# Kernel optimization log

Hardware: AMD Instinct MI355X
Metric: run time of the kernel (lower is better)

## Reference

```python
import jax, jax.numpy as jnp
import numpy as np

BATCH, LENGTH = 4, 512
D_MODEL, D_STATE, EXPAND = 128, 256, 2
D_INNER = EXPAND * D_MODEL  # 256 (== D_STATE, required by the original broadcasting)


def setup_inputs() -> dict:
    key = jax.random.key(0)
    ks = jax.random.split(key, 8)
    x = jax.random.normal(ks[0], (BATCH, LENGTH, D_MODEL), jnp.float32)
    # bias-free Dense kernels, fan-in scaled; W_delta and A kept small so
    # exp(delta*A)^L stays numerically tame over L=512 steps.
    W_in = jax.random.normal(ks[1], (D_MODEL, 2 * D_INNER), jnp.float32) / np.float32(np.sqrt(D_MODEL))
    W_delta = jax.random.normal(ks[2], (D_INNER, D_INNER), jnp.float32) * np.float32(0.005)
    W_B = jax.random.normal(ks[3], (D_INNER, D_STATE), jnp.float32) / np.float32(np.sqrt(D_INNER))
    W_C = jax.random.normal(ks[4], (D_INNER, D_INNER), jnp.float32) / np.float32(np.sqrt(D_INNER))
    W_out = jax.random.normal(ks[5], (D_INNER, D_MODEL), jnp.float32) / np.float32(np.sqrt(D_INNER))
    A = jax.random.normal(ks[6], (D_INNER, D_STATE), jnp.float32) * np.float32(0.02)
    D = jnp.ones((D_INNER,), jnp.float32)  # unused by the original scan, kept for faithfulness
    return dict(x=x, W_in=W_in, W_delta=W_delta, W_B=W_B, W_C=W_C, W_out=W_out, A=A, D=D)


def reference(x, W_in, W_delta, W_B, W_C, W_out, A, D):
    # in_proj + split
    x_proj = x @ W_in                      # (b, l, 2*d_inner)
    xs, z = jnp.split(x_proj, 2, axis=-1)  # each (b, l, d_inner)
    delta = xs @ W_delta                   # (b, l, d_inner)
    Bv = xs @ W_B                          # (b, l, d_state)
    Cv = xs @ W_C                          # (b, l, d_inner)

    # discretized transition/input, exactly as the original einsums
    deltaA = jnp.exp(jnp.einsum('bld,dn->bldn', delta, A))   # (b, l, d_inner, d_state)
    deltaB = jnp.einsum('bld,bln->bldn', delta, Bv)          # (b, l, d_inner, d_state)

    def step(state, inp):
        dA_i, dB_i, x_i, C_i = inp
        # state: (b, d_inner, d_state); x broadcast over the middle axis as in tf.expand_dims(x,1)
        state = dA_i * state + dB_i * x_i[:, None, :]
        y = jnp.einsum('bdn,bn->bd', state, C_i)
        return state, y

    init = jnp.zeros((x.shape[0], D_INNER, D_STATE), xs.dtype)
    inps = (
        jnp.moveaxis(deltaA, 1, 0),  # (l, b, d, n)
        jnp.moveaxis(deltaB, 1, 0),
        jnp.moveaxis(xs, 1, 0),      # (l, b, d)
        jnp.moveaxis(Cv, 1, 0),
    )
    _, ys = jax.lax.scan(step, init, inps)   # ys: (l, b, d_inner)
    y = jnp.moveaxis(ys, 0, 1)               # (b, l, d_inner)

    y = y * jax.nn.silu(z)
    return y @ W_out                          # (b, l, d_model)
```

## Files before the change

kernel.cpp:

```cpp
#include <hip/hip_runtime.h>
#include <hip/hip_bf16.h>


#define MROWS 2048
#define DM 128
#define DI 256
#define DS 256
#define LLEN 512
#define LC 64
#define NC 8

#define LOG2E 1.44269504088896340736f

typedef short bf16x8 __attribute__((ext_vector_type(8)));
typedef float f32x4  __attribute__((ext_vector_type(4)));

__device__ __forceinline__ short f2bf(float f) {
    union { float f; unsigned u; } v; v.f = f;
    unsigned r = v.u + 0x7FFFu + ((v.u >> 16) & 1u);
    return (short)(r >> 16);
}

#define TEXP2(c1, c2, dl) fmaf(fmaf((c2), (dl), (c1)), (dl), 1.f)

__device__ __forceinline__ void tconv(float (*tile)[33],
                                      const float* __restrict__ src,
                                      short* __restrict__ dst,
                                      int Ms, int Ns, int ti, int tj, int tid)
{
    const int r = tid >> 5, c = tid & 31;
#pragma unroll
    for (int i = 0; i < 4; ++i)
        tile[r + 8 * i][c] = src[(size_t)(ti * 32 + r + 8 * i) * Ns + tj * 32 + c];
    __syncthreads();
#pragma unroll
    for (int i = 0; i < 4; ++i)
        dst[(size_t)(tj * 32 + r + 8 * i) * Ms + ti * 32 + c] = f2bf(tile[c][r + 8 * i]);
}

__global__ __launch_bounds__(256) void k_proj_mfma(
    const float* __restrict__ x, const float* __restrict__ W_in,
    const float* __restrict__ Wd, const float* __restrict__ Wb,
    const float* __restrict__ Wc, const float* __restrict__ W_out,
    float* __restrict__ xs, short* __restrict__ xs_bf, float* __restrict__ sz,
    short* __restrict__ WdbcT, short* __restrict__ W_outT)
{
    const int t = threadIdx.x;

    if (blockIdx.x >= 8) {
        __shared__ float tile[32][33];
        const int uu = (blockIdx.x - 8) * 32 + blockIdx.y;
        if (uu < 64)       tconv(tile, Wd,    WdbcT,                       256, 256, uu & 7,         uu >> 3,         t);
        else if (uu < 128) tconv(tile, Wb,    WdbcT + (size_t)256 * 256,   256, 256, (uu - 64) & 7,  (uu - 64) >> 3,  t);
        else if (uu < 192) tconv(tile, Wc,    WdbcT + (size_t)512 * 256,   256, 256, (uu - 128) & 7, (uu - 128) >> 3, t);
        else if (uu < 224) tconv(tile, W_out, W_outT,                      256, 128, (uu - 192) & 7, (uu - 192) >> 3, t);
        return;
    }

    __shared__ short As[64][136];
    __shared__ short Bs[64][136];
    f32x4 acc[4] = {};
    const int w = t >> 6, lane = t & 63;
    const int srow = t >> 2, sseg = t & 3;
    const int frow = lane & 15, fk = (lane >> 4) << 3;
    const int r0 = blockIdx.y * 64, n0 = blockIdx.x * 64;

    {
        const float* ap = x + (size_t)(r0 + srow) * DM + sseg * 32;
        short tmp[32];
#pragma unroll
        for (int j = 0; j < 8; ++j) {
            float4 f = *(const float4*)(ap + j * 4);
            tmp[j * 4 + 0] = f2bf(f.x); tmp[j * 4 + 1] = f2bf(f.y);
            tmp[j * 4 + 2] = f2bf(f.z); tmp[j * 4 + 3] = f2bf(f.w);
        }
#pragma unroll
        for (int m = 0; m < 4; ++m)
            *(bf16x8*)&As[srow][sseg * 32 + m * 8] = *(bf16x8*)&tmp[m * 8];
    }
    {
#pragma unroll
        for (int i = 0; i < 32; i += 2) {
            const int k = sseg * 32 + i;
            float f0 = W_in[(size_t)k * 512 + n0 + srow];
            float f1 = W_in[(size_t)(k + 1) * 512 + n0 + srow];
            unsigned pk = (unsigned short)f2bf(f0) | ((unsigned)(unsigned short)f2bf(f1) << 16);
            *(unsigned*)&Bs[srow][k] = pk;
        }
    }
    __syncthreads();

#pragma unroll
    for (int kk = 0; kk < 128; kk += 32) {
        bf16x8 af = *(const bf16x8*)&As[w * 16 + frow][kk + fk];
#pragma unroll
        for (int ct = 0; ct < 4; ++ct) {
            bf16x8 bfr = *(const bf16x8*)&Bs[ct * 16 + frow][kk + fk];
            acc[ct] = __builtin_amdgcn_mfma_f32_16x16x32_bf16(af, bfr, acc[ct], 0, 0, 0);
        }
    }

    const int rr = r0 + w * 16 + (lane >> 4) * 4;
    const int c0 = n0 + (lane & 15);
#pragma unroll
    for (int ct = 0; ct < 4; ++ct) {
        const int c = c0 + ct * 16;
#pragma unroll
        for (int rg = 0; rg < 4; ++rg) {
            const float v = acc[ct][rg];
            const int r = rr + rg;
            if (c < DI) {
                xs[(size_t)r * DI + c]    = v;
                xs_bf[(size_t)r * DI + c] = f2bf(v);
            } else {
                sz[(size_t)r * DI + (c - DI)] = v / (1.f + __expf(-v));
            }
        }
    }
}

__global__ __launch_bounds__(512) void k_dbc(
    const short* __restrict__ xs_bf, const short* __restrict__ WdbcT,
    const float* __restrict__ xs,
    float* __restrict__ dlt, float* __restrict__ u, float* __restrict__ cvv)
{
    __shared__ short As[64][72], Bs[128][72];
    const int blk = blockIdx.x, t = threadIdx.x;
    const int w8 = t >> 6, lane = t & 63;
    const int rf = w8 & 3, ch = w8 >> 2;
    const int frow = lane & 15, fk = (lane >> 4) << 3;
    const int bx = blk % 6, by = blk / 6;
    const int r0 = by * 64, n0 = bx * 128;
    const int arow = t >> 3, ak = (t & 7) * 8;
    const int brow = t >> 2, bk = (t & 3) * 16;
    f32x4 acc[4] = {};

    for (int k0 = 0; k0 < DI; k0 += 64) {
        bf16x8 a0 = *(const bf16x8*)(xs_bf + (size_t)(r0 + arow) * DI + k0 + ak);
        bf16x8 b0 = *(const bf16x8*)(WdbcT + (size_t)(n0 + brow) * DI + k0 + bk);
        bf16x8 b1 = *(const bf16x8*)(WdbcT + (size_t)(n0 + brow) * DI + k0 + bk + 8);
        __syncthreads();
        *(bf16x8*)&As[arow][ak]     = a0;
        *(bf16x8*)&Bs[brow][bk]     = b0;
        *(bf16x8*)&Bs[brow][bk + 8] = b1;
        __syncthreads();
#pragma unroll
        for (int kk = 0; kk < 64; kk += 32) {
            bf16x8 af = *(const bf16x8*)&As[rf * 16 + frow][kk + fk];
#pragma unroll
            for (int ct = 0; ct < 4; ++ct) {
                bf16x8 bfr = *(const bf16x8*)&Bs[(ch * 4 + ct) * 16 + frow][kk + fk];
                acc[ct] = __builtin_amdgcn_mfma_f32_16x16x32_bf16(af, bfr, acc[ct], 0, 0, 0);
            }
        }
    }

    const int rr = r0 + rf * 16 + (lane >> 4) * 4;
    const int nbase = n0 + ch * 64;
    const int wsel = nbase >> 8;
    const int nb = nbase & 255;
#pragma unroll
    for (int ct = 0; ct < 4; ++ct) {
        const int c = nb + ct * 16 + (lane & 15);
#pragma unroll
        for (int rg = 0; rg < 4; ++rg) {
            const float v = acc[ct][rg];
            const size_t idx = (size_t)(rr + rg) * DI + c;
            if (wsel == 0)      dlt[idx] = v;
            else if (wsel == 1) u[idx]   = v * xs[idx];
            else                cvv[idx] = v;
        }
    }
}

__global__ __launch_bounds__(256) void k_scan1(
    const float* __restrict__ dlt, const float* __restrict__ u,
    const float* __restrict__ Aa,
    float* __restrict__ tc, float* __restrict__ dsm)
{
    const int lane = threadIdx.x & 63;
    const int w    = threadIdx.x >> 6;
    const int blk  = blockIdx.x;
    const int b  = blk & 3;
    const int c  = (blk >> 2) & 7;
    const int d0 = ((blk >> 5) * 4 + w) * 4;

    __shared__ float dls[4][4][LC];
    const size_t base = (size_t)b * LLEN * DI + (size_t)c * LC * DI;

    float4 dv = *(const float4*)(dlt + base + (size_t)lane * DI + d0);
    dls[w][0][lane] = dv.x;
    dls[w][1][lane] = dv.y;
    dls[w][2][lane] = dv.z;
    dls[w][3][lane] = dv.w;
    float dsv[4] = { dv.x, dv.y, dv.z, dv.w };
#pragma unroll
    for (int dd = 0; dd < 4; ++dd) {
#pragma unroll
        for (int off = 32; off > 0; off >>= 1)
            dsv[dd] += __shfl_xor(dsv[dd], off);
    }

    float4 c1[4], c2[4];
#pragma unroll
    for (int dd = 0; dd < 4; ++dd) {
        float4 a = *(const float4*)(Aa + (size_t)(d0 + dd) * DS + lane * 4);
        c1[dd] = a;
        c2[dd] = make_float4(0.5f * a.x * a.x, 0.5f * a.y * a.y,
                             0.5f * a.z * a.z, 0.5f * a.w * a.w);
    }

    const float4* up = (const float4*)(u + base) + lane;
    float4 s[4] = {};
    float4 uA[4], uB[4];

#define S1_PRE(UB, G)                                                         \
    {                                                                         \
        _Pragma("unroll")                                                     \
        for (int i = 0; i < 4; ++i)                                           \
            UB[i] = up[(size_t)((G) * 4 + i) * 64];                           \
    }

#define S1_COMP(UB, G)                                                        \
    {                                                                         \
        _Pragma("unroll")                                                     \
        for (int i = 0; i < 4; ++i) {                                         \
            const int l = (G) * 4 + i;                                        \
            _Pragma("unroll")                                                 \
            for (int dd = 0; dd < 4; ++dd) {                                  \
                const float dl = dls[w][dd][l];                               \
                s[dd].x = fmaf(TEXP2(c1[dd].x, c2[dd].x, dl), s[dd].x, dl * UB[i].x); \
                s[dd].y = fmaf(TEXP2(c1[dd].y, c2[dd].y, dl), s[dd].y, dl * UB[i].y); \
                s[dd].z = fmaf(TEXP2(c1[dd].z, c2[dd].z, dl), s[dd].z, dl * UB[i].z); \
                s[dd].w = fmaf(TEXP2(c1[dd].w, c2[dd].w, dl), s[dd].w, dl * UB[i].w); \
            }                                                                 \
        }                                                                     \
    }

    S1_PRE(uA, 0)
    for (int g2 = 0; g2 < 8; ++g2) {
        S1_PRE(uB, g2 * 2 + 1)
        S1_COMP(uA, g2 * 2)
        if (g2 < 7) S1_PRE(uA, g2 * 2 + 2)
        S1_COMP(uB, g2 * 2 + 1)
    }
#undef S1_PRE
#undef S1_COMP

    const size_t rbb = ((size_t)(b * 256 + d0)) * NC + c;
#pragma unroll
    for (int dd = 0; dd < 4; ++dd) {
        *(float4*)(tc + (rbb + (size_t)dd * NC) * 256 + lane * 4) = s[dd];
        if (lane == 0) dsm[rbb + dd * NC] = dsv[dd];
    }
}

__global__ __launch_bounds__(256) void k_scan3(
    const float* __restrict__ dlt, const float* __restrict__ u,
    const float* __restrict__ cvv, const float* __restrict__ Aa,
    const float* __restrict__ tc, const float* __restrict__ dsm,
    float* __restrict__ yv)
{
    const int lane = threadIdx.x & 63;
    const int w    = threadIdx.x >> 6;
    const int blk  = blockIdx.x;
    const int b  = blk & 3;
    const int c  = (blk >> 2) & 7;
    const int d0 = ((blk >> 5) * 4 + w) * 4;

    __shared__ float dls[4][4][LC];
    __shared__ float T[4][LC][20];

    const size_t base = (size_t)b * LLEN * DI + (size_t)c * LC * DI;

    float4 dv = *(const float4*)(dlt + base + (size_t)lane * DI + d0);
    dls[w][0][lane] = dv.x;
    dls[w][1][lane] = dv.y;
    dls[w][2][lane] = dv.z;
    dls[w][3][lane] = dv.w;

    float4 c1[4], c2[4];
#pragma unroll
    for (int dd = 0; dd < 4; ++dd) {
        float4 a = *(const float4*)(Aa + (size_t)(d0 + dd) * DS + lane * 4);
        c1[dd] = a;
        c2[dd] = make_float4(0.5f * a.x * a.x, 0.5f * a.y * a.y,
                             0.5f * a.z * a.z, 0.5f * a.w * a.w);
    }

    float4 s[4] = {};
    for (int cc = 0; cc < c; ++cc) {
#pragma unroll
        for (int dd = 0; dd < 4; ++dd) {
            const size_t rbd = ((size_t)(b * 256 + d0 + dd)) * NC + cc;
            const float4 Tt = *(const float4*)(tc + rbd * 256 + lane * 4);
            const float  Dc = dsm[rbd] * LOG2E;
            s[dd].x = exp2f(c1[dd].x * Dc) * s[dd].x + Tt.x;
            s[dd].y = exp2f(c1[dd].y * Dc) * s[dd].y + Tt.y;
            s[dd].z = exp2f(c1[dd].z * Dc) * s[dd].z + Tt.z;
            s[dd].w = exp2f(c1[dd].w * Dc) * s[dd].w + Tt.w;
        }
    }

    const float4* up = (const float4*)(u + base) + lane;
    const float4* cp = (const float4*)(cvv + base) + lane;
    float* yb = yv + base;

    const int col = lane & 15, seg = lane >> 4;
    float4 uA[4], cA[4], uB[4], cB[4];

#define S3_PRE(UB, CB, G)                                                     \
    {                                                                         \
        _Pragma("unroll")                                                     \
        for (int i = 0; i < 4; ++i) {                                         \
            UB[i] = up[(size_t)((G) * 4 + i) * 64];                           \
            CB[i] = cp[(size_t)((G) * 4 + i) * 64];                           \
        }                                                                     \
    }

#define S3_COMP(UB, CB, G)                                                    \
    {                                                                         \
        f32x4 pacc[4];                                                        \
        _Pragma("unroll")                                                     \
        for (int i = 0; i < 4; ++i) {                                         \
            const int l = (G) * 4 + i;                                        \
            _Pragma("unroll")                                                 \
            for (int dd = 0; dd < 4; ++dd) {                                  \
                const float dl = dls[w][dd][l];                               \
                s[dd].x = fmaf(TEXP2(c1[dd].x, c2[dd].x, dl), s[dd].x, dl * UB[i].x); \
                s[dd].y = fmaf(TEXP2(c1[dd].y, c2[dd].y, dl), s[dd].y, dl * UB[i].y); \
                s[dd].z = fmaf(TEXP2(c1[dd].z, c2[dd].z, dl), s[dd].z, dl * UB[i].z); \
                s[dd].w = fmaf(TEXP2(c1[dd].w, c2[dd].w, dl), s[dd].w, dl * UB[i].w); \
                pacc[dd][i] =                                                 \
                    fmaf(s[dd].w, CB[i].w, fmaf(s[dd].z, CB[i].z,             \
                         fmaf(s[dd].y, CB[i].y, s[dd].x * CB[i].x)));         \
            }                                                                 \
        }                                                                     \
        _Pragma("unroll")                                                     \
        for (int dd = 0; dd < 4; ++dd)                                        \
            *(f32x4*)&T[w][lane][dd * 4] = pacc[dd];                          \
        float sm = 0.f;                                                       \
        _Pragma("unroll")                                                     \
        for (int r = 0; r < 16; ++r)                                          \
            sm += T[w][seg * 16 + r][col];                                    \
        sm += __shfl_xor(sm, 16);                                             \
        sm += __shfl_xor(sm, 32);                                             \
        if (lane < 16)                                                        \
            yb[(size_t)((G) * 4 + (col & 3)) * DI + d0 + (col >> 2)] = sm;    \
    }

    S3_PRE(uA, cA, 0)
    for (int g2 = 0; g2 < 8; ++g2) {
        S3_PRE(uB, cB, g2 * 2 + 1)
        S3_COMP(uA, cA, g2 * 2)
        if (g2 < 7) S3_PRE(uA, cA, g2 * 2 + 2)
        S3_COMP(uB, cB, g2 * 2 + 1)
    }
#undef S3_PRE
#undef S3_COMP
}

__global__ __launch_bounds__(256) void k_out_mfma(
    const float* __restrict__ y, const float* __restrict__ szp,
    const short* __restrict__ W_outT, float* __restrict__ out)
{
    __shared__ short As[64][72], Bs[64][72];
    f32x4 acc[4] = {};
    const int tid  = threadIdx.x;
    const int w    = tid >> 6, lane = tid & 63;
    const int srow = tid >> 2, sseg = tid & 3;
    const int frow = lane & 15, fk = (lane >> 4) << 3;
    const int r0 = blockIdx.y * 64, n0 = blockIdx.x * 64;

    for (int k0 = 0; k0 < DI; k0 += 64) {
        const size_t aoff = (size_t)(r0 + srow) * DI + k0 + sseg * 16;
        float4 y0 = *(const float4*)(y + aoff);
        float4 y1 = *(const float4*)(y + aoff + 4);
        float4 y2 = *(const float4*)(y + aoff + 8);
        float4 y3 = *(const float4*)(y + aoff + 12);
        float4 s0 = *(const float4*)(szp + aoff);
        float4 s1 = *(const float4*)(szp + aoff + 4);
        float4 s2 = *(const float4*)(szp + aoff + 8);
        float4 s3 = *(const float4*)(szp + aoff + 12);
        const short* bg = W_outT + (size_t)(n0 + srow) * DI + k0 + sseg * 16;
        bf16x8 b0 = *(const bf16x8*)bg;
        bf16x8 b1 = *(const bf16x8*)(bg + 8);
        bf16x8 a0, a1;
        a0[0] = f2bf(y0.x * s0.x); a0[1] = f2bf(y0.y * s0.y);
        a0[2] = f2bf(y0.z * s0.z); a0[3] = f2bf(y0.w * s0.w);
        a0[4] = f2bf(y1.x * s1.x); a0[5] = f2bf(y1.y * s1.y);
        a0[6] = f2bf(y1.z * s1.z); a0[7] = f2bf(y1.w * s1.w);
        a1[0] = f2bf(y2.x * s2.x); a1[1] = f2bf(y2.y * s2.y);
        a1[2] = f2bf(y2.z * s2.z); a1[3] = f2bf(y2.w * s2.w);
        a1[4] = f2bf(y3.x * s3.x); a1[5] = f2bf(y3.y * s3.y);
        a1[6] = f2bf(y3.z * s3.z); a1[7] = f2bf(y3.w * s3.w);
        __syncthreads();
        *(bf16x8*)&As[srow][sseg * 16]     = a0;
        *(bf16x8*)&As[srow][sseg * 16 + 8] = a1;
        *(bf16x8*)&Bs[srow][sseg * 16]     = b0;
        *(bf16x8*)&Bs[srow][sseg * 16 + 8] = b1;
        __syncthreads();
#pragma unroll
        for (int kk = 0; kk < 64; kk += 32) {
            bf16x8 af = *(const bf16x8*)&As[w * 16 + frow][kk + fk];
#pragma unroll
            for (int ct = 0; ct < 4; ++ct) {
                bf16x8 bfr = *(const bf16x8*)&Bs[ct * 16 + frow][kk + fk];
                acc[ct] = __builtin_amdgcn_mfma_f32_16x16x32_bf16(af, bfr, acc[ct], 0, 0, 0);
            }
        }
    }

    const int rr = r0 + w * 16 + (lane >> 4) * 4;
    const int c0 = n0 + (lane & 15);
#pragma unroll
    for (int ct = 0; ct < 4; ++ct) {
        const int c = c0 + ct * 16;
#pragma unroll
        for (int rg = 0; rg < 4; ++rg)
            out[(size_t)(rr + rg) * DM + c] = acc[ct][rg];
    }
}

extern "C" void kernel_launch(void* const* d_in, const int* in_sizes, int n_in,
                              void* d_out, int out_size, void* d_ws, size_t ws_size,
                              hipStream_t stream)
{
    const float* x       = (const float*)d_in[0];
    const float* W_in    = (const float*)d_in[1];
    const float* W_delta = (const float*)d_in[2];
    const float* W_B     = (const float*)d_in[3];
    const float* W_C     = (const float*)d_in[4];
    const float* W_out   = (const float*)d_in[5];
    const float* A       = (const float*)d_in[6];

    float* out = (float*)d_out;
    float* ws  = (float*)d_ws;

    const size_t S = (size_t)MROWS * DI;
    float* xs  = ws;
    float* sz  = ws + S;
    float* dlt = ws + 2 * S;
    float* u   = ws + 3 * S;
    float* cv  = ws + 4 * S;
    float* yv  = ws + 5 * S;
    float* tc  = ws + 6 * S;
    float* dsm = tc + (size_t)1024 * NC * 256;

    short* xs_bf  = (short*)(dsm + (size_t)1024 * NC);
    short* WdbcT  = xs_bf + (size_t)MROWS * DI;
    short* W_outT = WdbcT + (size_t)768 * DI;

    k_proj_mfma<<<dim3(15, 32), 256, 0, stream>>>(x, W_in, W_delta, W_B, W_C, W_out,
                                                  xs, xs_bf, sz, WdbcT, W_outT);
    k_dbc      <<<dim3(192), 512, 0, stream>>>(xs_bf, WdbcT, xs, dlt, u, cv);
    k_scan1    <<<dim3(512), 256, 0, stream>>>(dlt, u, A, tc, dsm);
    k_scan3    <<<dim3(512), 256, 0, stream>>>(dlt, u, cv, A, tc, dsm, yv);
    k_out_mfma <<<dim3(2, 32), 256, 0, stream>>>(yv, sz, W_outT, out);
}
```

Measured before the change: 69.56 us.

## Fuse output projection into scan3 via last-block atomic counter, trim scan1 chunks

Drops the separate output-projection kernel. Each scan3 block bumps a per-(batch, chunk) atomic counter, and the 16th block to finish a chunk runs the gated bf16 MFMA projection for that chunk's 64 rows, reusing the T shared buffer as tiles. scan1 now launches 448 blocks covering only chunks 0-6, since the last chunk's carry summary is apparently unused, and scan1 resets the counters. This removes one launch and the kernel boundary, but the projection now runs on only a few tail blocks per chunk, serialising both output halves in one block, and it relies on the fences ordering yv correctly.

```diff
diff --git a/kernel.cpp b/kernel.cpp
--- a/kernel.cpp
+++ b/kernel.cpp
@@ -176,14 +176,18 @@
 __global__ __launch_bounds__(256) void k_scan1(
     const float* __restrict__ dlt, const float* __restrict__ u,
     const float* __restrict__ Aa,
-    float* __restrict__ tc, float* __restrict__ dsm)
+    float* __restrict__ tc, float* __restrict__ dsm,
+    unsigned* __restrict__ cnt)
 {
     const int lane = threadIdx.x & 63;
     const int w    = threadIdx.x >> 6;
     const int blk  = blockIdx.x;
     const int b  = blk & 3;
-    const int c  = (blk >> 2) & 7;
-    const int d0 = ((blk >> 5) * 4 + w) * 4;
+    const int r  = blk >> 2;
+    const int c  = r % 7;
+    const int d0 = ((r / 7) * 4 + w) * 4;
+
+    if (blk < 32 && threadIdx.x == 0) cnt[blk] = 0u;
 
     __shared__ float dls[4][4][LC];
     const size_t base = (size_t)b * LLEN * DI + (size_t)c * LC * DI;
@@ -259,7 +263,9 @@
     const float* __restrict__ dlt, const float* __restrict__ u,
     const float* __restrict__ cvv, const float* __restrict__ Aa,
     const float* __restrict__ tc, const float* __restrict__ dsm,
-    float* __restrict__ yv)
+    float* __restrict__ yv,
+    const float* __restrict__ szp, const short* __restrict__ W_outT,
+    float* __restrict__ out, unsigned* __restrict__ cnt)
 {
     const int lane = threadIdx.x & 63;
     const int w    = threadIdx.x >> 6;
@@ -270,6 +276,7 @@
 
     __shared__ float dls[4][4][LC];
     __shared__ float T[4][LC][20];
+    __shared__ bool  lastf;
 
     const size_t base = (size_t)b * LLEN * DI + (size_t)c * LC * DI;
 
@@ -358,67 +365,73 @@
     }
 #undef S3_PRE
 #undef S3_COMP
-}
-
-__global__ __launch_bounds__(256) void k_out_mfma(
-    const float* __restrict__ y, const float* __restrict__ szp,
-    const short* __restrict__ W_outT, float* __restrict__ out)
-{
-    __shared__ short As[64][72], Bs[64][72];
-    f32x4 acc[4] = {};
-    const int tid  = threadIdx.x;
-    const int w    = tid >> 6, lane = tid & 63;
-    const int srow = tid >> 2, sseg = tid & 3;
-    const int frow = lane & 15, fk = (lane >> 4) << 3;
-    const int r0 = blockIdx.y * 64, n0 = blockIdx.x * 64;
-
-    for (int k0 = 0; k0 < DI; k0 += 64) {
-        const size_t aoff = (size_t)(r0 + srow) * DI + k0 + sseg * 16;
-        float4 y0 = *(const float4*)(y + aoff);
-        float4 y1 = *(const float4*)(y + aoff + 4);
-        float4 y2 = *(const float4*)(y + aoff + 8);
-        float4 y3 = *(const float4*)(y + aoff + 12);
-        float4 s0 = *(const float4*)(szp + aoff);
-        float4 s1 = *(const float4*)(szp + aoff + 4);
-        float4 s2 = *(const float4*)(szp + aoff + 8);
-        float4 s3 = *(const float4*)(szp + aoff + 12);
-        const short* bg = W_outT + (size_t)(n0 + srow) * DI + k0 + sseg * 16;
-        bf16x8 b0 = *(const bf16x8*)bg;
-        bf16x8 b1 = *(const bf16x8*)(bg + 8);
-        bf16x8 a0, a1;
-        a0[0] = f2bf(y0.x * s0.x); a0[1] = f2bf(y0.y * s0.y);
-        a0[2] = f2bf(y0.z * s0.z); a0[3] = f2bf(y0.w * s0.w);
-        a0[4] = f2bf(y1.x * s1.x); a0[5] = f2bf(y1.y * s1.y);
-        a0[6] = f2bf(y1.z * s1.z); a0[7] = f2bf(y1.w * s1.w);
-        a1[0] = f2bf(y2.x * s2.x); a1[1] = f2bf(y2.y * s2.y);
-        a1[2] = f2bf(y2.z * s2.z); a1[3] = f2bf(y2.w * s2.w);
-        a1[4] = f2bf(y3.x * s3.x); a1[5] = f2bf(y3.y * s3.y);
-        a1[6] = f2bf(y3.z * s3.z); a1[7] = f2bf(y3.w * s3.w);
+
+    __threadfence();
+    if (threadIdx.x == 0)
+        lastf = (atomicAdd(&cnt[b * 8 + c], 1u) == 15u);
+    __syncthreads();
+    if (!lastf) return;
+    __threadfence();
+
+    short (*As)[72] = reinterpret_cast<short(*)[72]>(&T[0][0][0]);
+    short (*Bs)[72] = reinterpret_cast<short(*)[72]>(&T[0][0][0]) + 64;
+    const int r0f = b * 512 + c * 64;
+    const int t   = threadIdx.x;
+    const int ww  = t >> 6, ln = t & 63;
+    const int srow = t >> 2, sseg = t & 3;
+    const int frow = ln & 15, fk = (ln >> 4) << 3;
+
+    for (int half = 0; half < 2; ++half) {
+        const int n0 = half * 64;
+        f32x4 acc[4] = {};
+        for (int k0 = 0; k0 < DI; k0 += 64) {
+            const size_t aoff = (size_t)(r0f + srow) * DI + k0 + sseg * 16;
+            float4 y0 = *(const float4*)(yv + aoff);
+            float4 y1 = *(const float4*)(yv + aoff + 4);
+            float4 y2 = *(const float4*)(yv + aoff + 8);
+            float4 y3 = *(const float4*)(yv + aoff + 12);
+            float4 s0 = *(const float4*)(szp + aoff);
+            float4 s1 = *(const float4*)(szp + aoff + 4);
+            float4 s2 = *(const float4*)(szp + aoff + 8);
+            float4 s3 = *(const float4*)(szp + aoff + 12);
+            const short* bg = W_outT + (size_t)(n0 + srow) * DI + k0 + sseg * 16;
+            bf16x8 b0 = *(const bf16x8*)bg;
+            bf16x8 b1 = *(const bf16x8*)(bg + 8);
+            bf16x8 a0, a1;
+            a0[0] = f2bf(y0.x * s0.x); a0[1] = f2bf(y0.y * s0.y);
+            a0[2] = f2bf(y0.z * s0.z); a0[3] = f2bf(y0.w * s0.w);
+            a0[4] = f2bf(y1.x * s1.x); a0[5] = f2bf(y1.y * s1.y);
+            a0[6] = f2bf(y1.z * s1.z); a0[7] = f2bf(y1.w * s1.w);
+            a1[0] = f2bf(y2.x * s2.x); a1[1] = f2bf(y2.y * s2.y);
+            a1[2] = f2bf(y2.z * s2.z); a1[3] = f2bf(y2.w * s2.w);
+            a1[4] = f2bf(y3.x * s3.x); a1[5] = f2bf(y3.y * s3.y);
+            a1[6] = f2bf(y3.z * s3.z); a1[7] = f2bf(y3.w * s3.w);
+            __syncthreads();
+            *(bf16x8*)&As[srow][sseg * 16]     = a0;
+            *(bf16x8*)&As[srow][sseg * 16 + 8] = a1;
+            *(bf16x8*)&Bs[srow][sseg * 16]     = b0;
+            *(bf16x8*)&Bs[srow][sseg * 16 + 8] = b1;
+            __syncthreads();
+#pragma unroll
+            for (int kk = 0; kk < 64; kk += 32) {
+                bf16x8 af = *(const bf16x8*)&As[ww * 16 + frow][kk + fk];
+#pragma unroll
+                for (int ct = 0; ct < 4; ++ct) {
+                    bf16x8 bfr = *(const bf16x8*)&Bs[ct * 16 + frow][kk + fk];
+                    acc[ct] = __builtin_amdgcn_mfma_f32_16x16x32_bf16(af, bfr, acc[ct], 0, 0, 0);
+                }
+            }
+        }
+        const int rr = r0f + ww * 16 + (ln >> 4) * 4;
+        const int c0 = n0 + (ln & 15);
+#pragma unroll
+        for (int ct = 0; ct < 4; ++ct) {
+            const int cc = c0 + ct * 16;
+#pragma unroll
+            for (int rg = 0; rg < 4; ++rg)
+                out[(size_t)(rr + rg) * DM + cc] = acc[ct][rg];
+        }
         __syncthreads();
-        *(bf16x8*)&As[srow][sseg * 16]     = a0;
-        *(bf16x8*)&As[srow][sseg * 16 + 8] = a1;
-        *(bf16x8*)&Bs[srow][sseg * 16]     = b0;
-        *(bf16x8*)&Bs[srow][sseg * 16 + 8] = b1;
-        __syncthreads();
-#pragma unroll
-        for (int kk = 0; kk < 64; kk += 32) {
-            bf16x8 af = *(const bf16x8*)&As[w * 16 + frow][kk + fk];
-#pragma unroll
-            for (int ct = 0; ct < 4; ++ct) {
-                bf16x8 bfr = *(const bf16x8*)&Bs[ct * 16 + frow][kk + fk];
-                acc[ct] = __builtin_amdgcn_mfma_f32_16x16x32_bf16(af, bfr, acc[ct], 0, 0, 0);
-            }
-        }
-    }
-
-    const int rr = r0 + w * 16 + (lane >> 4) * 4;
-    const int c0 = n0 + (lane & 15);
-#pragma unroll
-    for (int ct = 0; ct < 4; ++ct) {
-        const int c = c0 + ct * 16;
-#pragma unroll
-        for (int rg = 0; rg < 4; ++rg)
-            out[(size_t)(rr + rg) * DM + c] = acc[ct][rg];
     }
 }
 
@@ -450,11 +463,12 @@
     short* xs_bf  = (short*)(dsm + (size_t)1024 * NC);
     short* WdbcT  = xs_bf + (size_t)MROWS * DI;
     short* W_outT = WdbcT + (size_t)768 * DI;
+    unsigned* cnt = (unsigned*)(W_outT + (size_t)128 * DI);
 
     k_proj_mfma<<<dim3(15, 32), 256, 0, stream>>>(x, W_in, W_delta, W_B, W_C, W_out,
                                                   xs, xs_bf, sz, WdbcT, W_outT);
     k_dbc      <<<dim3(192), 512, 0, stream>>>(xs_bf, WdbcT, xs, dlt, u, cv);
-    k_scan1    <<<dim3(512), 256, 0, stream>>>(dlt, u, A, tc, dsm);
-    k_scan3    <<<dim3(512), 256, 0, stream>>>(dlt, u, cv, A, tc, dsm, yv);
-    k_out_mfma <<<dim3(2, 32), 256, 0, stream>>>(yv, sz, W_outT, out);
-}
+    k_scan1    <<<dim3(448), 256, 0, stream>>>(dlt, u, A, tc, dsm, cnt);
+    k_scan3    <<<dim3(512), 256, 0, stream>>>(dlt, u, cv, A, tc, dsm, yv,
+                                               sz, W_outT, out, cnt);
+}
```

Result: slower. 121.2 us (+74.3%).
